# Performance work log

Measured on AMD Instinct MI355X. Metric: run time of the kernel, lower is better.

## Reference

```python
import jax, jax.numpy as jnp
import numpy as np

N, D, H, L, B, DFF = 100000, 256, 8, 64, 4096, 1024
HD = D // H  # head_dim
EPS = 1e-5


def _xavier(k, shape):
    lim = (6.0 / (shape[0] + shape[1])) ** 0.5
    return jax.random.uniform(k, shape, jnp.float32, -lim, lim)


def setup_inputs() -> dict:
    key = jax.random.key(0)
    ks = jax.random.split(key, 12)
    batch = jax.random.randint(ks[0], (B,), 0, N)
    nei_idx = jax.random.randint(ks[1], (B, L), 0, N)
    # faithful to neis_ = [[k] + neighbor[k] ...]: self node is first neighbor
    nei_idx = nei_idx.at[:, 0].set(batch)
    lengths = jax.random.randint(ks[2], (B,), 1, L + 1)
    nei_mask = jnp.arange(L)[None, :] >= lengths[:, None]  # True = NaN padding
    embeddings = jax.random.normal(ks[3], (N, D), jnp.float32)
    return {
        "batch": batch, "nei_idx": nei_idx, "nei_mask": nei_mask,
        "embeddings": embeddings,
        "Wq": _xavier(ks[4], (D, D)), "bq": jnp.zeros((D,), jnp.float32),
        "Wk": _xavier(ks[5], (D, D)), "bk": jnp.zeros((D,), jnp.float32),
        "Wv": _xavier(ks[6], (D, D)), "bv": jnp.zeros((D,), jnp.float32),
        "Wo": _xavier(ks[7], (D, D)), "bo": jnp.zeros((D,), jnp.float32),
        "W1": _xavier(ks[8], (D, DFF)), "b1": jnp.zeros((DFF,), jnp.float32),
        "W2": _xavier(ks[9], (DFF, D)), "b2": jnp.zeros((D,), jnp.float32),
        "ln1_w": jnp.ones((D,), jnp.float32), "ln1_b": jnp.zeros((D,), jnp.float32),
        "ln2_w": jnp.ones((D,), jnp.float32), "ln2_b": jnp.zeros((D,), jnp.float32),
    }


def _layer_norm(y, w, b):
    mu = y.mean(-1, keepdims=True)
    var = ((y - mu) ** 2).mean(-1, keepdims=True)
    return (y - mu) / jnp.sqrt(var + EPS) * w + b


def reference(batch, nei_idx, nei_mask, embeddings,
              Wq, bq, Wk, bk, Wv, bv, Wo, bo,
              W1, b1, W2, b2, ln1_w, ln1_b, ln2_w, ln2_b):
    x = embeddings[batch]        # [B, D]  query-node embeddings
    nei = embeddings[nei_idx]    # [B, L, D] gathered (padded) neighbor embeds
    q = ((x @ Wq + bq) * (HD ** -0.5)).reshape(B, H, HD)
    k = (nei @ Wk + bk).reshape(B, L, H, HD)
    v = (nei @ Wv + bv).reshape(B, L, H, HD)
    scores = jnp.einsum('bhd,blhd->bhl', q, k)          # single-query attn
    scores = jnp.where(nei_mask[:, None, :], -jnp.inf, scores)
    att = jax.nn.softmax(scores, axis=-1)               # [B, H, L]
    attout = jnp.einsum('bhl,blhd->bhd', att, v).reshape(B, D) @ Wo + bo
    s = _layer_norm(x + attout, ln1_w, ln1_b)
    # note: original applies relu after BOTH linear1 and linear2
    f = jax.nn.relu(jax.nn.relu(s @ W1 + b1) @ W2 + b2)
    return _layer_norm(s + f, ln2_w, ln2_b)
```

## Files before the change

### kernel.cpp

```cpp
#include <hip/hip_runtime.h>
#include <hip/hip_bf16.h>
#include <math.h>

#define BQ   4096
#define D    256
#define NH   8
#define HD   32
#define LN_  64
#define DFF  1024
#define EPSV 1e-5f
#define QSCALE 0.17677669529663687f

typedef __attribute__((ext_vector_type(8))) short short8;
typedef __attribute__((ext_vector_type(4))) float f32x4;

#define ESWZ(row, byte) ((byte) ^ (((row) & 7) << 4))

__device__ __forceinline__ float wave_sum(float v){
#pragma unroll
  for (int off = 32; off; off >>= 1) v += __shfl_xor(v, off, 64);
  return v;
}
__device__ __forceinline__ unsigned short f2bf(float f){
  unsigned int u = __float_as_uint(f);
  unsigned int r = (u + 0x7FFFu + ((u >> 16) & 1u)) >> 16;
  return (unsigned short)r;
}

__global__ __launch_bounds__(256) void k_prep(
    const float* __restrict__ Wq, const float* __restrict__ Wk,
    const float* __restrict__ Wv, const float* __restrict__ Wo,
    const float* __restrict__ W1, const float* __restrict__ W2,
    const float* __restrict__ bq, const float* __restrict__ bv,
    const float* __restrict__ bo,
    const int* __restrict__ batch, const float* __restrict__ emb,
    const unsigned int* __restrict__ maskw,
    unsigned short* __restrict__ W1t, unsigned short* __restrict__ W2t,
    unsigned short* __restrict__ Mt, unsigned short* __restrict__ Gt,
    float* __restrict__ pb, float* __restrict__ bo2,
    float* __restrict__ X, unsigned short* __restrict__ Xb,
    int* __restrict__ flags){
  __shared__ float smem[4224];
  const int bid = blockIdx.x;
  const int tid = threadIdx.x;

  if (bid < 128){
    const float* src; unsigned short* dst; int K, N, t0;
    if (bid < 64){ src = W1; dst = W1t; K = 256;  N = 1024; t0 = bid; }
    else         { src = W2; dst = W2t; K = 1024; N = 256;  t0 = bid - 64; }
    const int ntx = N / 64;
    const int k0 = (t0 / ntx) * 64, n0 = (t0 % ntx) * 64;
    float (*Ts)[65] = (float(*)[65])smem;
    {
      int r = tid >> 2, c4 = (tid & 3) * 16;
#pragma unroll
      for (int i = 0; i < 4; i++)
        *(float4*)&Ts[r][c4 + i * 4] = *(const float4*)(src + (size_t)(k0 + r) * N + n0 + c4 + i * 4);
    }
    __syncthreads();
    {
      int n = tid >> 2, kc = (tid & 3) * 16;
      unsigned int pk[8];
#pragma unroll
      for (int i = 0; i < 8; i++){
        unsigned int lo = f2bf(Ts[kc + 2 * i][n]);
        unsigned int hi = f2bf(Ts[kc + 2 * i + 1][n]);
        pk[i] = lo | (hi << 16);
      }
      unsigned short* orow = dst + (size_t)(n0 + n) * K + k0 + kc;
      *(uint4*)(orow)     = *(uint4*)&pk[0];
      *(uint4*)(orow + 8) = *(uint4*)&pk[4];
    }
    return;
  }
  if (bid < 256){
    int t0 = bid - 128;
    int hd0 = (t0 & 31) * 64, c0 = (t0 >> 5) * 64;
    int h = hd0 >> 8, d0 = hd0 & 255;
    float (*WqS)[33] = (float(*)[33])smem;
    float (*WkS)[33] = (float(*)[33])(smem + 64 * 33);
#pragma unroll
    for (int s = 0; s < 2; s++){
      int idx = tid + s * 256;
      int row = idx >> 3, c4 = (idx & 7) * 4;
      *(float4*)&WqS[row][c4] = *(const float4*)(Wq + (size_t)(c0 + row) * 256 + h * 32 + c4);
      *(float4*)&WkS[row][c4] = *(const float4*)(Wk + (size_t)(d0 + row) * 256 + h * 32 + c4);
    }
    __syncthreads();
    int jo = (tid >> 4) * 4, io = (tid & 15) * 4;
    float acc[4][4];
#pragma unroll
    for (int j = 0; j < 4; j++)
#pragma unroll
      for (int i = 0; i < 4; i++) acc[j][i] = 0.f;
#pragma unroll
    for (int t = 0; t < 32; t++){
#pragma unroll
      for (int j = 0; j < 4; j++){
        float kv = WkS[jo + j][t];
#pragma unroll
        for (int i = 0; i < 4; i++) acc[j][i] = fmaf(kv, WqS[io + i][t], acc[j][i]);
      }
    }
#pragma unroll
    for (int j = 0; j < 4; j++){
      uint2 o;
      o.x = (unsigned)f2bf(acc[j][0] * QSCALE) | ((unsigned)f2bf(acc[j][1] * QSCALE) << 16);
      o.y = (unsigned)f2bf(acc[j][2] * QSCALE) | ((unsigned)f2bf(acc[j][3] * QSCALE) << 16);
      *(uint2*)(Mt + (size_t)(hd0 + jo + j) * 256 + c0 + io) = o;
    }
    if (c0 == 0 && tid < 64){
      float s = 0.f;
#pragma unroll
      for (int t = 0; t < 32; t++) s = fmaf(WkS[tid][t], bq[h * 32 + t], s);
      pb[hd0 + tid] = s * QSCALE;
    }
    return;
  }
  if (bid < 384){
    int t0 = bid - 256;
    int hd0 = (t0 & 31) * 64, n0 = (t0 >> 5) * 64;
    int h = hd0 >> 8, d0 = hd0 & 255;
    float (*WvS)[33] = (float(*)[33])smem;
    float (*WoS)[65] = (float(*)[65])(smem + 64 * 33);
#pragma unroll
    for (int s = 0; s < 2; s++){
      int idx = tid + s * 256;
      int row = idx >> 3, c4 = (idx & 7) * 4;
      *(float4*)&WvS[row][c4] = *(const float4*)(Wv + (size_t)(d0 + row) * 256 + h * 32 + c4);
      int row2 = idx >> 4, c42 = (idx & 15) * 4;
      *(float4*)&WoS[row2][c42] = *(const float4*)(Wo + (size_t)(h * 32 + row2) * 256 + n0 + c42);
    }
    __syncthreads();
    int jo = (tid >> 4) * 4, io = (tid & 15) * 4;
    float acc[4][4];
#pragma unroll
    for (int i = 0; i < 4; i++)
#pragma unroll
      for (int j = 0; j < 4; j++) acc[i][j] = 0.f;
#pragma unroll
    for (int t = 0; t < 32; t++){
#pragma unroll
      for (int i = 0; i < 4; i++){
        float ov = WoS[t][io + i];
#pragma unroll
        for (int j = 0; j < 4; j++) acc[i][j] = fmaf(ov, WvS[jo + j][t], acc[i][j]);
      }
    }
#pragma unroll
    for (int i = 0; i < 4; i++){
      uint2 o;
      o.x = (unsigned)f2bf(acc[i][0]) | ((unsigned)f2bf(acc[i][1]) << 16);
      o.y = (unsigned)f2bf(acc[i][2]) | ((unsigned)f2bf(acc[i][3]) << 16);
      *(uint2*)(Gt + (size_t)(n0 + io + i) * 2048 + hd0 + jo) = o;
    }
    return;
  }
  if (bid == 384){
    int n = tid;
    float s = bo[n];
    for (int j = 0; j < 256; j++) s = fmaf(bv[j], Wo[(size_t)j * 256 + n], s);
    bo2[n] = s;
    return;
  }
  if (bid < 641){
    int idx = (bid - 385) * 256 + tid;
    unsigned int v = maskw[idx];
    int bits = 0;
    if (v == 0x3F800000u) bits = 2;
    else if (v & 0xFFFFFF00u) bits = 1;
    int b2 = __any(bits & 2) ? 2 : 0;
    int b1 = __any(bits & 1) ? 1 : 0;
    if ((tid & 63) == 0 && (b1 | b2)) atomicOr(flags, b1 | b2);
    return;
  }
  {
    int gid = (bid - 641) * 256 + tid;
    int b = gid >> 6, c = gid & 63;
    float4 v = ((const float4*)(emb + (size_t)batch[b] * D))[c];
    ((float4*)(X + (size_t)b * D))[c] = v;
    uint2 p;
    p.x = (unsigned)f2bf(v.x) | ((unsigned)f2bf(v.y) << 16);
    p.y = (unsigned)f2bf(v.z) | ((unsigned)f2bf(v.w) << 16);
    ((uint2*)Xb)[gid] = p;
  }
}

template<int BM, int BN, int EPI, bool OUTBF>
__global__ __launch_bounds__(256) void k_mgemm(const unsigned short* __restrict__ A,
                                               const unsigned short* __restrict__ Bt,
                                               const float* __restrict__ bias,
                                               void* __restrict__ Cout,
                                               int M, int N, int K){
  constexpr int BK = 64;
  constexpr int WM = BM / 2, WN = BN / 2;
  constexpr int MR = WM / 16, NR = WN / 16;
  __shared__ __align__(16) unsigned short As[BM * BK];
  __shared__ __align__(16) unsigned short Bs[BN * BK];
  char* ab = (char*)As; char* bb = (char*)Bs;
  const int tid = threadIdx.x;
  const int w = tid >> 6, lane = tid & 63;
  const int wm = w >> 1, wn = w & 1;
  const int row0 = blockIdx.y * BM, col0 = blockIdx.x * BN;
  f32x4 acc[MR][NR];
#pragma unroll
  for (int m = 0; m < MR; m++)
#pragma unroll
    for (int n = 0; n < NR; n++) acc[m][n] = (f32x4){0.f, 0.f, 0.f, 0.f};

  constexpr int AIT = BM * 8 / 256;
  constexpr int BIT = BN * 8 / 256;

  for (int k0 = 0; k0 < K; k0 += BK){
#pragma unroll
    for (int s = 0; s < AIT; s++){
      int c = s * 256 + tid;
      int r = c >> 3, jj = c & 7;
      uint4 v = *(const uint4*)(A + (size_t)(row0 + r) * K + k0 + jj * 8);
      *(uint4*)(ab + ESWZ(r, r * 128 + jj * 16)) = v;
    }
#pragma unroll
    for (int s = 0; s < BIT; s++){
      int c = s * 256 + tid;
      int r = c >> 3, jj = c & 7;
      uint4 v = *(const uint4*)(Bt + (size_t)(col0 + r) * K + k0 + jj * 8);
      *(uint4*)(bb + ESWZ(r, r * 128 + jj * 16)) = v;
    }
    __syncthreads();
#pragma unroll
    for (int kk = 0; kk < 2; kk++){
      short8 af[MR], bf[NR];
#pragma unroll
      for (int m = 0; m < MR; m++){
        int r = wm * WM + m * 16 + (lane & 15);
        af[m] = *(const short8*)(ab + ESWZ(r, r * 128 + (kk * 4 + (lane >> 4)) * 16));
      }
#pragma unroll
      for (int n = 0; n < NR; n++){
        int r = wn * WN + n * 16 + (lane & 15);
        bf[n] = *(const short8*)(bb + ESWZ(r, r * 128 + (kk * 4 + (lane >> 4)) * 16));
      }
#pragma unroll
      for (int m = 0; m < MR; m++)
#pragma unroll
        for (int n = 0; n < NR; n++)
          acc[m][n] = __builtin_amdgcn_mfma_f32_16x16x32_bf16(af[m], bf[n], acc[m][n], 0, 0, 0);
    }
    __syncthreads();
  }
#pragma unroll
  for (int m = 0; m < MR; m++){
#pragma unroll
    for (int n = 0; n < NR; n++){
      int col = col0 + wn * WN + n * 16 + (lane & 15);
      float bsv = bias[col];
      int rbase = row0 + wm * WM + m * 16 + (lane >> 4) * 4;
#pragma unroll
      for (int r = 0; r < 4; r++){
        float v = acc[m][n][r] + bsv;
        if (EPI == 3) v = fmaxf(v, 0.f);
        if (OUTBF) ((unsigned short*)Cout)[(size_t)(rbase + r) * N + col] = f2bf(v);
        else       ((float*)Cout)[(size_t)(rbase + r) * N + col] = v;
      }
    }
  }
}

__global__ __launch_bounds__(256) void k_attn(const int* __restrict__ nei_idx,
                                              const void* __restrict__ nei_mask,
                                              const int* __restrict__ flagp,
                                              const float* __restrict__ emb,
                                              const unsigned short* __restrict__ Pb,
                                              unsigned short* __restrict__ Cb){
  const int b = blockIdx.x;
  const int tid = threadIdx.x;
  const int w = tid >> 6, lane = tid & 63;
  __shared__ __align__(16) unsigned short Ebf[64 * 256];
  __shared__ __align__(16) unsigned short Pl[9 * 256];
  __shared__ float sc[NH * LN_];
  __shared__ int   nid[LN_];
  __shared__ float mskv[LN_];
  char* eb = (char*)Ebf;
  char* pl = (char*)Pl;

  const int fl = flagp[0];
  const int mf = (fl & 2) ? 2 : ((fl & 1) ? 1 : 0);
  if (tid < LN_){
    nid[tid] = nei_idx[(size_t)b * LN_ + tid];
    bool m;
    if (mf == 1)      m = ((const unsigned char*)nei_mask)[(size_t)b * LN_ + tid] != 0;
    else if (mf == 2) m = ((const float*)nei_mask)[(size_t)b * LN_ + tid] != 0.f;
    else              m = ((const int*)nei_mask)[(size_t)b * LN_ + tid] != 0;
    mskv[tid] = m ? 1.f : 0.f;
  }
  {
    int r = tid >> 5, cb16 = (tid & 31) * 16;
    uint4 v = *(const uint4*)((const char*)Pb + (size_t)b * 4096 + r * 512 + cb16);
    *(uint4*)(pl + ESWZ(r, r * 512 + cb16)) = v;
    if (tid < 64) *(uint2*)(pl + 8 * 512 + tid * 8) = make_uint2(0u, 0u);
  }
  __syncthreads();

#pragma unroll
  for (int half = 0; half < 2; half++){
    float4 vr[8];
#pragma unroll
    for (int i = 0; i < 8; i++){
      int l = w * 16 + half * 8 + i;
      vr[i] = ((const float4*)(emb + (size_t)nid[l] * D))[lane];
    }
#pragma unroll
    for (int i = 0; i < 8; i++){
      int l = w * 16 + half * 8 + i;
      uint2 p;
      p.x = (unsigned)f2bf(vr[i].x) | ((unsigned)f2bf(vr[i].y) << 16);
      p.y = (unsigned)f2bf(vr[i].z) | ((unsigned)f2bf(vr[i].w) << 16);
      *(uint2*)(eb + ESWZ(l, l * 512 + lane * 8)) = p;
    }
  }
  __syncthreads();

  {
    const int hr = lane & 15;
    const int arow = hr < 8 ? hr : 8;
    const int bl = w * 16 + (lane & 15);
    const int koff = (lane >> 4) * 16;
    f32x4 acc = {0.f, 0.f, 0.f, 0.f};
#pragma unroll
    for (int kk = 0; kk < 8; kk++){
      short8 af = *(const short8*)(pl + ESWZ(arow, arow * 512 + kk * 64 + koff));
      short8 bf = *(const short8*)(eb + ESWZ(bl, bl * 512 + kk * 64 + koff));
      acc = __builtin_amdgcn_mfma_f32_16x16x32_bf16(af, bf, acc, 0, 0, 0);
    }
    int l = w * 16 + (lane & 15);
    int hb = (lane >> 4) * 4;
    if (hb < 8){
#pragma unroll
      for (int r = 0; r < 4; r++) sc[(hb + r) * LN_ + l] = acc[r];
    }
  }
  __syncthreads();

  {
    int h = tid >> 5, j = tid & 31;
    float v0 = mskv[j]      > 0.5f ? -INFINITY : sc[h * LN_ + j];
    float v1 = mskv[j + 32] > 0.5f ? -INFINITY : sc[h * LN_ + j + 32];
    float m = fmaxf(v0, v1);
#pragma unroll
    for (int off = 16; off; off >>= 1) m = fmaxf(m, __shfl_xor(m, off, 64));
    float e0 = __expf(v0 - m), e1 = __expf(v1 - m);
    float s = e0 + e1;
#pragma unroll
    for (int off = 16; off; off >>= 1) s += __shfl_xor(s, off, 64);
    float inv = 1.f / s;
    sc[h * LN_ + j]      = e0 * inv;
    sc[h * LN_ + j + 32] = e1 * inv;
  }
  __syncthreads();

  {
    const int h0 = w * 2, h1 = w * 2 + 1;
    float4 a0 = make_float4(0.f, 0.f, 0.f, 0.f);
    float4 a1 = make_float4(0.f, 0.f, 0.f, 0.f);
#pragma unroll 8
    for (int l = 0; l < 64; l++){
      uint2 raw = *(const uint2*)(eb + ESWZ(l, l * 512 + lane * 8));
      float e0 = __uint_as_float(raw.x << 16);
      float e1 = __uint_as_float(raw.x & 0xFFFF0000u);
      float e2 = __uint_as_float(raw.y << 16);
      float e3 = __uint_as_float(raw.y & 0xFFFF0000u);
      float t0 = sc[h0 * LN_ + l], t1 = sc[h1 * LN_ + l];
      a0.x = fmaf(t0, e0, a0.x); a0.y = fmaf(t0, e1, a0.y);
      a0.z = fmaf(t0, e2, a0.z); a0.w = fmaf(t0, e3, a0.w);
      a1.x = fmaf(t1, e0, a1.x); a1.y = fmaf(t1, e1, a1.y);
      a1.z = fmaf(t1, e2, a1.z); a1.w = fmaf(t1, e3, a1.w);
    }
    uint2 o0, o1;
    o0.x = (unsigned)f2bf(a0.x) | ((unsigned)f2bf(a0.y) << 16);
    o0.y = (unsigned)f2bf(a0.z) | ((unsigned)f2bf(a0.w) << 16);
    o1.x = (unsigned)f2bf(a1.x) | ((unsigned)f2bf(a1.y) << 16);
    o1.y = (unsigned)f2bf(a1.z) | ((unsigned)f2bf(a1.w) << 16);
    *(uint2*)((char*)Cb + (size_t)b * 4096 + h0 * 512 + lane * 8) = o0;
    *(uint2*)((char*)Cb + (size_t)b * 4096 + h1 * 512 + lane * 8) = o1;
  }
}

__global__ __launch_bounds__(256) void k_ln(const float* __restrict__ A,
                                            const float* __restrict__ Bv,
                                            const float* __restrict__ w,
                                            const float* __restrict__ bi,
                                            float* __restrict__ out,
                                            unsigned short* __restrict__ outb){
  const int row = blockIdx.x, tid = threadIdx.x;
  const int wv = tid >> 6, lane = tid & 63;
  __shared__ float red[8];
  float v = A[(size_t)row * D + tid] + Bv[(size_t)row * D + tid];
  float s = wave_sum(v);
  if (lane == 0) red[wv] = s;
  __syncthreads();
  float mu = (red[0] + red[1] + red[2] + red[3]) * (1.f / D);
  float d = v - mu;
  float s2 = wave_sum(d * d);
  if (lane == 0) red[4 + wv] = s2;
  __syncthreads();
  float var = (red[4] + red[5] + red[6] + red[7]) * (1.f / D);
  float res = d * rsqrtf(var + EPSV) * w[tid] + bi[tid];
  out[(size_t)row * D + tid] = res;
  if (outb) outb[(size_t)row * D + tid] = f2bf(res);
}

extern "C" void kernel_launch(void* const* d_in, const int* in_sizes, int n_in,
                              void* d_out, int out_size, void* d_ws, size_t ws_size,
                              hipStream_t stream){
  (void)in_sizes; (void)n_in; (void)out_size; (void)ws_size;
  const int*   batch    = (const int*)d_in[0];
  const int*   nei_idx  = (const int*)d_in[1];
  const void*  nei_mask = d_in[2];
  const float* emb      = (const float*)d_in[3];
  const float* Wq = (const float*)d_in[4];  const float* bq = (const float*)d_in[5];
  const float* Wk = (const float*)d_in[6];
  const float* Wv = (const float*)d_in[8];  const float* bv = (const float*)d_in[9];
  const float* Wo = (const float*)d_in[10]; const float* bo = (const float*)d_in[11];
  const float* W1 = (const float*)d_in[12]; const float* b1 = (const float*)d_in[13];
  const float* W2 = (const float*)d_in[14]; const float* b2 = (const float*)d_in[15];
  const float* ln1w = (const float*)d_in[16]; const float* ln1b = (const float*)d_in[17];
  const float* ln2w = (const float*)d_in[18]; const float* ln2b = (const float*)d_in[19];

  float* ws = (float*)d_ws;
  float* X  = ws;
  float* Y  = ws + (size_t)1 * 1048576;
  float* S  = ws + (size_t)2 * 1048576;
  float* F  = ws + (size_t)3 * 1048576;
  unsigned short* Pbf = (unsigned short*)(ws + (size_t)4 * 1048576);
  unsigned short* Cb  = Pbf;
  unsigned short* Sb  = (unsigned short*)(ws + (size_t)8 * 1048576);
  unsigned short* HHb = (unsigned short*)(ws + (size_t)9 * 1048576);
  unsigned short* Xb  = (unsigned short*)(ws + (size_t)11 * 1048576);
  char* wb = (char*)(ws + (size_t)12 * 1048576);
  unsigned short* W1t = (unsigned short*)(wb);
  unsigned short* W2t = (unsigned short*)(wb + (512u << 10));
  unsigned short* Mt  = (unsigned short*)(wb + (1024u << 10));
  unsigned short* Gt  = (unsigned short*)(wb + (2048u << 10));
  float* pbv  = (float*)(wb + (3072u << 10));
  float* bo2  = (float*)(wb + (3072u << 10) + 8192);
  int*   flags = (int*)(wb + (3072u << 10) + 16384);
  float* out = (float*)d_out;

  hipMemsetAsync(flags, 0, 4, stream);
  k_prep<<<1665, 256, 0, stream>>>(Wq, Wk, Wv, Wo, W1, W2, bq, bv, bo,
                                   batch, emb, (const unsigned int*)nei_mask,
                                   W1t, W2t, Mt, Gt, pbv, bo2, X, Xb, flags);
  k_mgemm<128, 64, 2, true><<<dim3(2048 / 64, BQ / 128), 256, 0, stream>>>(Xb, Mt, pbv, Pbf, BQ, 2048, 256);
  k_attn<<<BQ, 256, 0, stream>>>(nei_idx, nei_mask, flags, emb, Pbf, Cb);
  k_mgemm<64, 64, 2, false><<<dim3(D / 64, BQ / 64), 256, 0, stream>>>(Cb, Gt, bo2, Y, BQ, D, 2048);
  k_ln<<<BQ, 256, 0, stream>>>(X, Y, ln1w, ln1b, S, Sb);
  k_mgemm<128, 64, 3, true><<<dim3(DFF / 64, BQ / 128), 256, 0, stream>>>(Sb, W1t, b1, HHb, BQ, DFF, 256);
  k_mgemm<64, 64, 3, false><<<dim3(D / 64, BQ / 64), 256, 0, stream>>>(HHb, W2t, b2, F, BQ, D, DFF);
  k_ln<<<BQ, 256, 0, stream>>>(S, F, ln2w, ln2b, out, nullptr);
}
```

Measured before the change: 132.4 us.

## Prefetch GEMM tiles into registers, widen attention blocks, drop flag memset

The GEMM kernel now loads the next K tile into registers while computing the current tile from shared memory, hiding some global-load latency. The attention kernel moves to 512 threads per query. The score MFMA is split across K-halves and summed, and each wave handles one head for softmax and the weighted sum. The global atomic mask flag and its memset are replaced by per-block flag slots that each attention block reduces, which removes one launch but adds 256 flag reads per attention block.

```diff
diff --git a/kernel.cpp b/kernel.cpp
--- a/kernel.cpp
+++ b/kernel.cpp
@@ -39,7 +39,7 @@
     unsigned short* __restrict__ Mt, unsigned short* __restrict__ Gt,
     float* __restrict__ pb, float* __restrict__ bo2,
     float* __restrict__ X, unsigned short* __restrict__ Xb,
-    int* __restrict__ flags){
+    int* __restrict__ flagsArr){
   __shared__ float smem[4224];
   const int bid = blockIdx.x;
   const int tid = threadIdx.x;
@@ -164,6 +164,9 @@
     return;
   }
   if (bid < 641){
+    int* df = (int*)smem;
+    if (tid == 0) df[0] = 0;
+    __syncthreads();
     int idx = (bid - 385) * 256 + tid;
     unsigned int v = maskw[idx];
     int bits = 0;
@@ -171,7 +174,9 @@
     else if (v & 0xFFFFFF00u) bits = 1;
     int b2 = __any(bits & 2) ? 2 : 0;
     int b1 = __any(bits & 1) ? 1 : 0;
-    if ((tid & 63) == 0 && (b1 | b2)) atomicOr(flags, b1 | b2);
+    if ((tid & 63) == 0 && (b1 | b2)) atomicOr(df, b1 | b2);
+    __syncthreads();
+    if (tid == 0) flagsArr[bid - 385] = df[0];
     return;
   }
   {
@@ -195,6 +200,8 @@
   constexpr int BK = 64;
   constexpr int WM = BM / 2, WN = BN / 2;
   constexpr int MR = WM / 16, NR = WN / 16;
+  constexpr int AIT = BM * 8 / 256;
+  constexpr int BIT = BN * 8 / 256;
   __shared__ __align__(16) unsigned short As[BM * BK];
   __shared__ __align__(16) unsigned short Bs[BN * BK];
   char* ab = (char*)As; char* bb = (char*)Bs;
@@ -208,25 +215,36 @@
 #pragma unroll
     for (int n = 0; n < NR; n++) acc[m][n] = (f32x4){0.f, 0.f, 0.f, 0.f};
 
-  constexpr int AIT = BM * 8 / 256;
-  constexpr int BIT = BN * 8 / 256;
-
-  for (int k0 = 0; k0 < K; k0 += BK){
+  uint4 avr[AIT], bvr[BIT];
+  auto load_tiles = [&](int k0){
 #pragma unroll
     for (int s = 0; s < AIT; s++){
       int c = s * 256 + tid;
       int r = c >> 3, jj = c & 7;
-      uint4 v = *(const uint4*)(A + (size_t)(row0 + r) * K + k0 + jj * 8);
-      *(uint4*)(ab + ESWZ(r, r * 128 + jj * 16)) = v;
+      avr[s] = *(const uint4*)(A + (size_t)(row0 + r) * K + k0 + jj * 8);
     }
 #pragma unroll
     for (int s = 0; s < BIT; s++){
       int c = s * 256 + tid;
       int r = c >> 3, jj = c & 7;
-      uint4 v = *(const uint4*)(Bt + (size_t)(col0 + r) * K + k0 + jj * 8);
-      *(uint4*)(bb + ESWZ(r, r * 128 + jj * 16)) = v;
-    }
-    __syncthreads();
+      bvr[s] = *(const uint4*)(Bt + (size_t)(col0 + r) * K + k0 + jj * 8);
+    }
+  };
+  auto store_tiles = [&](){
+#pragma unroll
+    for (int s = 0; s < AIT; s++){
+      int c = s * 256 + tid;
+      int r = c >> 3, jj = c & 7;
+      *(uint4*)(ab + ESWZ(r, r * 128 + jj * 16)) = avr[s];
+    }
+#pragma unroll
+    for (int s = 0; s < BIT; s++){
+      int c = s * 256 + tid;
+      int r = c >> 3, jj = c & 7;
+      *(uint4*)(bb + ESWZ(r, r * 128 + jj * 16)) = bvr[s];
+    }
+  };
+  auto compute = [&](){
 #pragma unroll
     for (int kk = 0; kk < 2; kk++){
       short8 af[MR], bf[NR];
@@ -246,8 +264,20 @@
         for (int n = 0; n < NR; n++)
           acc[m][n] = __builtin_amdgcn_mfma_f32_16x16x32_bf16(af[m], bf[n], acc[m][n], 0, 0, 0);
     }
-    __syncthreads();
-  }
+  };
+
+  load_tiles(0);
+  store_tiles();
+  __syncthreads();
+  for (int k0 = BK; k0 < K; k0 += BK){
+    load_tiles(k0);
+    compute();
+    __syncthreads();
+    store_tiles();
+    __syncthreads();
+  }
+  compute();
+
 #pragma unroll
   for (int m = 0; m < MR; m++){
 #pragma unroll
@@ -266,9 +296,9 @@
   }
 }
 
-__global__ __launch_bounds__(256) void k_attn(const int* __restrict__ nei_idx,
+__global__ __launch_bounds__(512) void k_attn(const int* __restrict__ nei_idx,
                                               const void* __restrict__ nei_mask,
-                                              const int* __restrict__ flagp,
+                                              const int* __restrict__ flagsArr,
                                               const float* __restrict__ emb,
                                               const unsigned short* __restrict__ Pb,
                                               unsigned short* __restrict__ Cb){
@@ -277,16 +307,31 @@
   const int w = tid >> 6, lane = tid & 63;
   __shared__ __align__(16) unsigned short Ebf[64 * 256];
   __shared__ __align__(16) unsigned short Pl[9 * 256];
-  __shared__ float sc[NH * LN_];
+  __shared__ float sc[2 * NH * LN_];
   __shared__ int   nid[LN_];
   __shared__ float mskv[LN_];
+  __shared__ int   fred[4];
   char* eb = (char*)Ebf;
   char* pl = (char*)Pl;
 
-  const int fl = flagp[0];
-  const int mf = (fl & 2) ? 2 : ((fl & 1) ? 1 : 0);
+  if (tid < LN_) nid[tid] = nei_idx[(size_t)b * LN_ + tid];
+  if (tid < 256){
+    int f = flagsArr[tid];
+#pragma unroll
+    for (int off = 32; off; off >>= 1) f |= __shfl_xor(f, off, 64);
+    if (lane == 0) fred[w] = f;
+  }
+  if (tid < 256){
+    int r = tid >> 5, cb16 = (tid & 31) * 16;
+    uint4 v = *(const uint4*)((const char*)Pb + (size_t)b * 4096 + r * 512 + cb16);
+    *(uint4*)(pl + ESWZ(r, r * 512 + cb16)) = v;
+  }
+  if (tid < 64) *(uint2*)(pl + 8 * 512 + tid * 8) = make_uint2(0u, 0u);
+  __syncthreads();
+
   if (tid < LN_){
-    nid[tid] = nei_idx[(size_t)b * LN_ + tid];
+    int fl = fred[0] | fred[1] | fred[2] | fred[3];
+    int mf = (fl & 2) ? 2 : ((fl & 1) ? 1 : 0);
     bool m;
     if (mf == 1)      m = ((const unsigned char*)nei_mask)[(size_t)b * LN_ + tid] != 0;
     else if (mf == 2) m = ((const float*)nei_mask)[(size_t)b * LN_ + tid] != 0.f;
@@ -294,24 +339,15 @@
     mskv[tid] = m ? 1.f : 0.f;
   }
   {
-    int r = tid >> 5, cb16 = (tid & 31) * 16;
-    uint4 v = *(const uint4*)((const char*)Pb + (size_t)b * 4096 + r * 512 + cb16);
-    *(uint4*)(pl + ESWZ(r, r * 512 + cb16)) = v;
-    if (tid < 64) *(uint2*)(pl + 8 * 512 + tid * 8) = make_uint2(0u, 0u);
-  }
-  __syncthreads();
-
-#pragma unroll
-  for (int half = 0; half < 2; half++){
     float4 vr[8];
 #pragma unroll
     for (int i = 0; i < 8; i++){
-      int l = w * 16 + half * 8 + i;
+      int l = w * 8 + i;
       vr[i] = ((const float4*)(emb + (size_t)nid[l] * D))[lane];
     }
 #pragma unroll
     for (int i = 0; i < 8; i++){
-      int l = w * 16 + half * 8 + i;
+      int l = w * 8 + i;
       uint2 p;
       p.x = (unsigned)f2bf(vr[i].x) | ((unsigned)f2bf(vr[i].y) << 16);
       p.y = (unsigned)f2bf(vr[i].z) | ((unsigned)f2bf(vr[i].w) << 16);
@@ -323,65 +359,54 @@
   {
     const int hr = lane & 15;
     const int arow = hr < 8 ? hr : 8;
-    const int bl = w * 16 + (lane & 15);
+    const int bl = (w & 3) * 16 + (lane & 15);
+    const int kh = w >> 2;
     const int koff = (lane >> 4) * 16;
     f32x4 acc = {0.f, 0.f, 0.f, 0.f};
 #pragma unroll
-    for (int kk = 0; kk < 8; kk++){
-      short8 af = *(const short8*)(pl + ESWZ(arow, arow * 512 + kk * 64 + koff));
-      short8 bf = *(const short8*)(eb + ESWZ(bl, bl * 512 + kk * 64 + koff));
+    for (int kk = 0; kk < 4; kk++){
+      int kabs = kh * 4 + kk;
+      short8 af = *(const short8*)(pl + ESWZ(arow, arow * 512 + kabs * 64 + koff));
+      short8 bf = *(const short8*)(eb + ESWZ(bl, bl * 512 + kabs * 64 + koff));
       acc = __builtin_amdgcn_mfma_f32_16x16x32_bf16(af, bf, acc, 0, 0, 0);
     }
-    int l = w * 16 + (lane & 15);
     int hb = (lane >> 4) * 4;
     if (hb < 8){
 #pragma unroll
-      for (int r = 0; r < 4; r++) sc[(hb + r) * LN_ + l] = acc[r];
+      for (int r = 0; r < 4; r++) sc[kh * 512 + (hb + r) * LN_ + bl] = acc[r];
     }
   }
   __syncthreads();
 
   {
-    int h = tid >> 5, j = tid & 31;
-    float v0 = mskv[j]      > 0.5f ? -INFINITY : sc[h * LN_ + j];
-    float v1 = mskv[j + 32] > 0.5f ? -INFINITY : sc[h * LN_ + j + 32];
-    float m = fmaxf(v0, v1);
-#pragma unroll
-    for (int off = 16; off; off >>= 1) m = fmaxf(m, __shfl_xor(m, off, 64));
-    float e0 = __expf(v0 - m), e1 = __expf(v1 - m);
-    float s = e0 + e1;
-#pragma unroll
-    for (int off = 16; off; off >>= 1) s += __shfl_xor(s, off, 64);
-    float inv = 1.f / s;
-    sc[h * LN_ + j]      = e0 * inv;
-    sc[h * LN_ + j + 32] = e1 * inv;
+    float v = sc[w * LN_ + lane] + sc[512 + w * LN_ + lane];
+    v = mskv[lane] > 0.5f ? -INFINITY : v;
+    float m = v;
+#pragma unroll
+    for (int off = 32; off; off >>= 1) m = fmaxf(m, __shfl_xor(m, off, 64));
+    float e = __expf(v - m);
+    float s = e;
+#pragma unroll
+    for (int off = 32; off; off >>= 1) s += __shfl_xor(s, off, 64);
+    sc[w * LN_ + lane] = e / s;
   }
   __syncthreads();
 
   {
-    const int h0 = w * 2, h1 = w * 2 + 1;
     float4 a0 = make_float4(0.f, 0.f, 0.f, 0.f);
-    float4 a1 = make_float4(0.f, 0.f, 0.f, 0.f);
 #pragma unroll 8
     for (int l = 0; l < 64; l++){
       uint2 raw = *(const uint2*)(eb + ESWZ(l, l * 512 + lane * 8));
-      float e0 = __uint_as_float(raw.x << 16);
-      float e1 = __uint_as_float(raw.x & 0xFFFF0000u);
-      float e2 = __uint_as_float(raw.y << 16);
-      float e3 = __uint_as_float(raw.y & 0xFFFF0000u);
-      float t0 = sc[h0 * LN_ + l], t1 = sc[h1 * LN_ + l];
-      a0.x = fmaf(t0, e0, a0.x); a0.y = fmaf(t0, e1, a0.y);
-      a0.z = fmaf(t0, e2, a0.z); a0.w = fmaf(t0, e3, a0.w);
-      a1.x = fmaf(t1, e0, a1.x); a1.y = fmaf(t1, e1, a1.y);
-      a1.z = fmaf(t1, e2, a1.z); a1.w = fmaf(t1, e3, a1.w);
-    }
-    uint2 o0, o1;
+      float t0 = sc[w * LN_ + l];
+      a0.x = fmaf(t0, __uint_as_float(raw.x << 16), a0.x);
+      a0.y = fmaf(t0, __uint_as_float(raw.x & 0xFFFF0000u), a0.y);
+      a0.z = fmaf(t0, __uint_as_float(raw.y << 16), a0.z);
+      a0.w = fmaf(t0, __uint_as_float(raw.y & 0xFFFF0000u), a0.w);
+    }
+    uint2 o0;
     o0.x = (unsigned)f2bf(a0.x) | ((unsigned)f2bf(a0.y) << 16);
     o0.y = (unsigned)f2bf(a0.z) | ((unsigned)f2bf(a0.w) << 16);
-    o1.x = (unsigned)f2bf(a1.x) | ((unsigned)f2bf(a1.y) << 16);
-    o1.y = (unsigned)f2bf(a1.z) | ((unsigned)f2bf(a1.w) << 16);
-    *(uint2*)((char*)Cb + (size_t)b * 4096 + h0 * 512 + lane * 8) = o0;
-    *(uint2*)((char*)Cb + (size_t)b * 4096 + h1 * 512 + lane * 8) = o1;
+    *(uint2*)((char*)Cb + (size_t)b * 4096 + w * 512 + lane * 8) = o0;
   }
 }
 
@@ -443,15 +468,14 @@
   unsigned short* Gt  = (unsigned short*)(wb + (2048u << 10));
   float* pbv  = (float*)(wb + (3072u << 10));
   float* bo2  = (float*)(wb + (3072u << 10) + 8192);
-  int*   flags = (int*)(wb + (3072u << 10) + 16384);
+  int*   flagsArr = (int*)(wb + (3072u << 10) + 16384);
   float* out = (float*)d_out;
 
-  hipMemsetAsync(flags, 0, 4, stream);
   k_prep<<<1665, 256, 0, stream>>>(Wq, Wk, Wv, Wo, W1, W2, bq, bv, bo,
                                    batch, emb, (const unsigned int*)nei_mask,
-                                   W1t, W2t, Mt, Gt, pbv, bo2, X, Xb, flags);
+                                   W1t, W2t, Mt, Gt, pbv, bo2, X, Xb, flagsArr);
   k_mgemm<128, 64, 2, true><<<dim3(2048 / 64, BQ / 128), 256, 0, stream>>>(Xb, Mt, pbv, Pbf, BQ, 2048, 256);
-  k_attn<<<BQ, 256, 0, stream>>>(nei_idx, nei_mask, flags, emb, Pbf, Cb);
+  k_attn<<<BQ, 512, 0, stream>>>(nei_idx, nei_mask, flagsArr, emb, Pbf, Cb);
   k_mgemm<64, 64, 2, false><<<dim3(D / 64, BQ / 64), 256, 0, stream>>>(Cb, Gt, bo2, Y, BQ, D, 2048);
   k_ln<<<BQ, 256, 0, stream>>>(X, Y, ln1w, ln1b, S, Sb);
   k_mgemm<128, 64, 3, true><<<dim3(DFF / 64, BQ / 128), 256, 0, stream>>>(Sb, W1t, b1, HHb, BQ, DFF, 256);
```

New measurement: 226.8 us. +71.3%, slower.

## Per-block mask flags, XCD-aware GEMM tile remap, hoisted attn gathers, smaller GEMM tiles

Applied to the files above, without the earlier changes.

Mask-dtype detection now writes one flag per block into an array instead of using a global atomic, and the attention kernel OR-reduces those flags, so the memset is no longer needed. The GEMM kernel remaps workgroup IDs in groups of eight, intended to spread neighbouring tiles across XCDs for better L2 locality. The attention kernel issues all 16 neighbor embedding gathers per wave up front, before the first barrier, to get more loads in flight. The two narrow-N GEMMs switch to 32-row tiles to launch more workgroups. The trade-offs are higher register pressure in attention and less operand reuse per GEMM tile.

```diff
diff --git a/kernel.cpp b/kernel.cpp
--- a/kernel.cpp
+++ b/kernel.cpp
@@ -39,7 +39,7 @@
     unsigned short* __restrict__ Mt, unsigned short* __restrict__ Gt,
     float* __restrict__ pb, float* __restrict__ bo2,
     float* __restrict__ X, unsigned short* __restrict__ Xb,
-    int* __restrict__ flags){
+    int* __restrict__ flagsArr){
   __shared__ float smem[4224];
   const int bid = blockIdx.x;
   const int tid = threadIdx.x;
@@ -164,6 +164,9 @@
     return;
   }
   if (bid < 641){
+    int* df = (int*)smem;
+    if (tid == 0) df[0] = 0;
+    __syncthreads();
     int idx = (bid - 385) * 256 + tid;
     unsigned int v = maskw[idx];
     int bits = 0;
@@ -171,7 +174,9 @@
     else if (v & 0xFFFFFF00u) bits = 1;
     int b2 = __any(bits & 2) ? 2 : 0;
     int b1 = __any(bits & 1) ? 1 : 0;
-    if ((tid & 63) == 0 && (b1 | b2)) atomicOr(flags, b1 | b2);
+    if ((tid & 63) == 0 && (b1 | b2)) atomicOr(df, b1 | b2);
+    __syncthreads();
+    if (tid == 0) flagsArr[bid - 385] = df[0];
     return;
   }
   {
@@ -195,21 +200,24 @@
   constexpr int BK = 64;
   constexpr int WM = BM / 2, WN = BN / 2;
   constexpr int MR = WM / 16, NR = WN / 16;
+  constexpr int AIT = BM * 8 / 256;
+  constexpr int BIT = BN * 8 / 256;
   __shared__ __align__(16) unsigned short As[BM * BK];
   __shared__ __align__(16) unsigned short Bs[BN * BK];
   char* ab = (char*)As; char* bb = (char*)Bs;
   const int tid = threadIdx.x;
   const int w = tid >> 6, lane = tid & 63;
   const int wm = w >> 1, wn = w & 1;
-  const int row0 = blockIdx.y * BM, col0 = blockIdx.x * BN;
+  const int gx = gridDim.x;
+  const int nwg = gx * gridDim.y;
+  const int o = blockIdx.y * gx + blockIdx.x;
+  const int lin = (o & 7) * (nwg >> 3) + (o >> 3);
+  const int row0 = (lin / gx) * BM, col0 = (lin % gx) * BN;
   f32x4 acc[MR][NR];
 #pragma unroll
   for (int m = 0; m < MR; m++)
 #pragma unroll
     for (int n = 0; n < NR; n++) acc[m][n] = (f32x4){0.f, 0.f, 0.f, 0.f};
-
-  constexpr int AIT = BM * 8 / 256;
-  constexpr int BIT = BN * 8 / 256;
 
   for (int k0 = 0; k0 < K; k0 += BK){
 #pragma unroll
@@ -268,7 +276,7 @@
 
 __global__ __launch_bounds__(256) void k_attn(const int* __restrict__ nei_idx,
                                               const void* __restrict__ nei_mask,
-                                              const int* __restrict__ flagp,
+                                              const int* __restrict__ flagsArr,
                                               const float* __restrict__ emb,
                                               const unsigned short* __restrict__ Pb,
                                               unsigned short* __restrict__ Cb){
@@ -278,46 +286,48 @@
   __shared__ __align__(16) unsigned short Ebf[64 * 256];
   __shared__ __align__(16) unsigned short Pl[9 * 256];
   __shared__ float sc[NH * LN_];
-  __shared__ int   nid[LN_];
   __shared__ float mskv[LN_];
+  __shared__ int   fred[4];
   char* eb = (char*)Ebf;
   char* pl = (char*)Pl;
 
-  const int fl = flagp[0];
-  const int mf = (fl & 2) ? 2 : ((fl & 1) ? 1 : 0);
+  {
+    int f = flagsArr[tid];
+#pragma unroll
+    for (int off = 32; off; off >>= 1) f |= __shfl_xor(f, off, 64);
+    if (lane == 0) fred[w] = f;
+  }
+  float4 vr[16];
+#pragma unroll
+  for (int i = 0; i < 16; i++){
+    int nid = nei_idx[(size_t)b * LN_ + w * 16 + i];
+    vr[i] = ((const float4*)(emb + (size_t)nid * D))[lane];
+  }
+  {
+    int r = tid >> 5, cb16 = (tid & 31) * 16;
+    uint4 v = *(const uint4*)((const char*)Pb + (size_t)b * 4096 + r * 512 + cb16);
+    *(uint4*)(pl + ESWZ(r, r * 512 + cb16)) = v;
+  }
+  if (tid < 64) *(uint2*)(pl + 8 * 512 + tid * 8) = make_uint2(0u, 0u);
+  __syncthreads();
+
+#pragma unroll
+  for (int i = 0; i < 16; i++){
+    int l = w * 16 + i;
+    uint2 p;
+    p.x = (unsigned)f2bf(vr[i].x) | ((unsigned)f2bf(vr[i].y) << 16);
+    p.y = (unsigned)f2bf(vr[i].z) | ((unsigned)f2bf(vr[i].w) << 16);
+    *(uint2*)(eb + ESWZ(l, l * 512 + lane * 8)) = p;
+  }
   if (tid < LN_){
-    nid[tid] = nei_idx[(size_t)b * LN_ + tid];
+    int fl = fred[0] | fred[1] | fred[2] | fred[3];
+    int mf = (fl & 2) ? 2 : ((fl & 1) ? 1 : 0);
     bool m;
     if (mf == 1)      m = ((const unsigned char*)nei_mask)[(size_t)b * LN_ + tid] != 0;
     else if (mf == 2) m = ((const float*)nei_mask)[(size_t)b * LN_ + tid] != 0.f;
     else              m = ((const int*)nei_mask)[(size_t)b * LN_ + tid] != 0;
     mskv[tid] = m ? 1.f : 0.f;
   }
-  {
-    int r = tid >> 5, cb16 = (tid & 31) * 16;
-    uint4 v = *(const uint4*)((const char*)Pb + (size_t)b * 4096 + r * 512 + cb16);
-    *(uint4*)(pl + ESWZ(r, r * 512 + cb16)) = v;
-    if (tid < 64) *(uint2*)(pl + 8 * 512 + tid * 8) = make_uint2(0u, 0u);
-  }
-  __syncthreads();
-
-#pragma unroll
-  for (int half = 0; half < 2; half++){
-    float4 vr[8];
-#pragma unroll
-    for (int i = 0; i < 8; i++){
-      int l = w * 16 + half * 8 + i;
-      vr[i] = ((const float4*)(emb + (size_t)nid[l] * D))[lane];
-    }
-#pragma unroll
-    for (int i = 0; i < 8; i++){
-      int l = w * 16 + half * 8 + i;
-      uint2 p;
-      p.x = (unsigned)f2bf(vr[i].x) | ((unsigned)f2bf(vr[i].y) << 16);
-      p.y = (unsigned)f2bf(vr[i].z) | ((unsigned)f2bf(vr[i].w) << 16);
-      *(uint2*)(eb + ESWZ(l, l * 512 + lane * 8)) = p;
-    }
-  }
   __syncthreads();
 
   {
@@ -332,11 +342,10 @@
       short8 bf = *(const short8*)(eb + ESWZ(bl, bl * 512 + kk * 64 + koff));
       acc = __builtin_amdgcn_mfma_f32_16x16x32_bf16(af, bf, acc, 0, 0, 0);
     }
-    int l = w * 16 + (lane & 15);
     int hb = (lane >> 4) * 4;
     if (hb < 8){
 #pragma unroll
-      for (int r = 0; r < 4; r++) sc[(hb + r) * LN_ + l] = acc[r];
+      for (int r = 0; r < 4; r++) sc[(hb + r) * LN_ + bl] = acc[r];
     }
   }
   __syncthreads();
@@ -443,18 +452,17 @@
   unsigned short* Gt  = (unsigned short*)(wb + (2048u << 10));
   float* pbv  = (float*)(wb + (3072u << 10));
   float* bo2  = (float*)(wb + (3072u << 10) + 8192);
-  int*   flags = (int*)(wb + (3072u << 10) + 16384);
+  int*   flagsArr = (int*)(wb + (3072u << 10) + 16384);
   float* out = (float*)d_out;
 
-  hipMemsetAsync(flags, 0, 4, stream);
   k_prep<<<1665, 256, 0, stream>>>(Wq, Wk, Wv, Wo, W1, W2, bq, bv, bo,
                                    batch, emb, (const unsigned int*)nei_mask,
-                                   W1t, W2t, Mt, Gt, pbv, bo2, X, Xb, flags);
+                                   W1t, W2t, Mt, Gt, pbv, bo2, X, Xb, flagsArr);
   k_mgemm<128, 64, 2, true><<<dim3(2048 / 64, BQ / 128), 256, 0, stream>>>(Xb, Mt, pbv, Pbf, BQ, 2048, 256);
-  k_attn<<<BQ, 256, 0, stream>>>(nei_idx, nei_mask, flags, emb, Pbf, Cb);
-  k_mgemm<64, 64, 2, false><<<dim3(D / 64, BQ / 64), 256, 0, stream>>>(Cb, Gt, bo2, Y, BQ, D, 2048);
+  k_attn<<<BQ, 256, 0, stream>>>(nei_idx, nei_mask, flagsArr, emb, Pbf, Cb);
+  k_mgemm<32, 64, 2, false><<<dim3(D / 64, BQ / 32), 256, 0, stream>>>(Cb, Gt, bo2, Y, BQ, D, 2048);
   k_ln<<<BQ, 256, 0, stream>>>(X, Y, ln1w, ln1b, S, Sb);
   k_mgemm<128, 64, 3, true><<<dim3(DFF / 64, BQ / 128), 256, 0, stream>>>(Sb, W1t, b1, HHb, BQ, DFF, 256);
-  k_mgemm<64, 64, 3, false><<<dim3(D / 64, BQ / 64), 256, 0, stream>>>(HHb, W2t, b2, F, BQ, D, DFF);
+  k_mgemm<32, 64, 3, false><<<dim3(D / 64, BQ / 32), 256, 0, stream>>>(HHb, W2t, b2, F, BQ, D, DFF);
   k_ln<<<BQ, 256, 0, stream>>>(S, F, ln2w, ln2b, out, nullptr);
 }
```

Result: faster. 122.3 us (-7.6%).
